# Kernel tuning notes

Measured on AMD Instinct MI355X. Metric: run time of the kernel, lower is better.

Reference implementation:

```python
import jax, jax.numpy as jnp
import numpy as np
import math
from jax import lax

BATCH, SEQ_LEN, ENC_IN = 8, 2048, 1
D_MODEL, N_HEADS, E_LAYERS, D_FF, FACTOR, C_OUT = 512, 8, 3, 512, 5, 2
EPS = 1e-5


def _layernorm(x, g, b):
    mu = x.mean(-1, keepdims=True)
    var = ((x - mu) ** 2).mean(-1, keepdims=True)
    return (x - mu) / jnp.sqrt(var + EPS) * g + b


def _prob_attention(q, k, v, key):
    # q,k,v: [B,H,L,Dh]; ProbSparse: sample U keys per query, pick top-u queries by M = max - mean
    B, H, L, Dh = q.shape
    U = min(FACTOR * int(np.ceil(np.log(L))), L)  # U_part == u since L_Q == L_K
    idx = jax.random.randint(key, (L, U), 0, L)   # sampled key indices per query
    k_samp = k[:, :, idx, :]                       # [B,H,L,U,Dh]
    qk = jnp.einsum('bhld,bhlud->bhlu', q, k_samp)
    M = qk.max(-1) - qk.mean(-1)                   # sparsity measure [B,H,L]
    _, top = lax.top_k(M, U)                       # active query indices [B,H,U]
    q_red = jnp.take_along_axis(q, top[..., None], axis=2)
    scores = jnp.einsum('bhud,bhkd->bhuk', q_red, k) * (1.0 / math.sqrt(Dh))
    A = jax.nn.softmax(scores, axis=-1)
    ctx = jnp.broadcast_to(v.mean(axis=2, keepdims=True), q.shape)  # lazy-query context = mean(V)
    upd = jnp.einsum('bhuk,bhkd->bhud', A, v)
    b = jnp.arange(B)[:, None, None]
    h = jnp.arange(H)[None, :, None]
    return ctx.at[b, h, top].set(upd)


def _encoder_layer(x, p, key):
    Wq, Wk, Wv, bq, bk, bv, Wo, bo, W1, b1, W2, b2, g1, be1, g2, be2 = p
    B, L, dm = x.shape
    Dh = dm // N_HEADS
    split = lambda t: t.reshape(B, L, N_HEADS, Dh).transpose(0, 2, 1, 3)
    q = split(x @ Wq.T + bq)
    k = split(x @ Wk.T + bk)
    v = split(x @ Wv.T + bv)
    o = _prob_attention(q, k, v, key).transpose(0, 2, 1, 3).reshape(B, L, dm)
    x = _layernorm(x + o @ Wo.T + bo, g1, be1)
    y = jax.nn.gelu(x @ W1.T + b1, approximate=False) @ W2.T + b2  # 1x1 convs == linears
    return _layernorm(x + y, g2, be2)


def _distil_conv(x, w, b, g, be):
    # Conv1d(dm,dm,3, circular pad) -> BatchNorm(eval) -> ELU -> MaxPool1d(3, stride 2, pad 1)
    xc = jnp.pad(x.transpose(0, 2, 1), ((0, 0), (0, 0), (1, 1)), mode='wrap')
    y = lax.conv_general_dilated(xc, w, (1,), 'VALID', dimension_numbers=('NCH', 'OIH', 'NCH'))
    y = y + b[None, :, None]
    y = y / np.float32(np.sqrt(1.0 + EPS)) * g[None, :, None] + be[None, :, None]
    y = jax.nn.elu(y)
    y = lax.reduce_window(y, -jnp.inf, lax.max, (1, 1, 3), (1, 1, 2), [(0, 0), (0, 0), (1, 1)])
    return y.transpose(0, 2, 1)


def _forward(x_enc, tok_w, Wq, Wk, Wv, bq, bk, bv, Wo, bo, W1, b1, W2, b2,
             ln1_g, ln1_b, ln2_g, ln2_b, dc_w, dc_b, bn_g, bn_b, lnf_g, lnf_b, proj_w, proj_b):
    B, L = x_enc.shape
    dm = D_MODEL
    # TokenEmbedding: circular Conv1d(1, d_model, 3, bias=False)
    xc = jnp.pad(x_enc[:, None, :], ((0, 0), (0, 0), (1, 1)), mode='wrap')
    tok = lax.conv_general_dilated(xc, tok_w, (1,), 'VALID', dimension_numbers=('NCH', 'OIH', 'NCH'))
    tok = tok.transpose(0, 2, 1)  # [B,L,dm]
    # fixed sinusoidal positional embedding
    pos = jnp.arange(L, dtype=jnp.float32)[:, None]
    div = jnp.exp(jnp.arange(0, dm, 2, dtype=jnp.float32) * (-math.log(10000.0) / dm))
    pe = jnp.zeros((L, dm), jnp.float32).at[:, 0::2].set(jnp.sin(pos * div)).at[:, 1::2].set(jnp.cos(pos * div))
    x = tok + pe[None]
    key = jax.random.key(42)
    for i in range(E_LAYERS):
        p = (Wq[i], Wk[i], Wv[i], bq[i], bk[i], bv[i], Wo[i], bo[i],
             W1[i], b1[i], W2[i], b2[i], ln1_g[i], ln1_b[i], ln2_g[i], ln2_b[i])
        x = _encoder_layer(x, p, jax.random.fold_in(key, i))
        if i < E_LAYERS - 1:
            x = _distil_conv(x, dc_w[i], dc_b[i], bn_g[i], bn_b[i])
    x = _layernorm(x, lnf_g, lnf_b)
    return x.max(axis=1) @ proj_w.T + proj_b  # [B, C_OUT]


def setup_inputs() -> dict:
    key = jax.random.key(0)
    ks = jax.random.split(key, 12)
    dm, dff, L = D_MODEL, D_FF, E_LAYERS
    w = lambda k, shape, fan: jax.random.normal(k, shape, jnp.float32) / np.float32(np.sqrt(fan))
    return {
        'x_enc': jax.random.normal(ks[0], (BATCH, SEQ_LEN), jnp.float32),
        'tok_w': w(ks[1], (dm, ENC_IN, 3), 3 * ENC_IN),
        'Wq': w(ks[2], (L, dm, dm), dm), 'Wk': w(ks[3], (L, dm, dm), dm),
        'Wv': w(ks[4], (L, dm, dm), dm), 'Wo': w(ks[5], (L, dm, dm), dm),
        'bq': jnp.zeros((L, dm)), 'bk': jnp.zeros((L, dm)),
        'bv': jnp.zeros((L, dm)), 'bo': jnp.zeros((L, dm)),
        'W1': w(ks[6], (L, dff, dm), dm), 'b1': jnp.zeros((L, dff)),
        'W2': w(ks[7], (L, dm, dff), dff), 'b2': jnp.zeros((L, dm)),
        'ln1_g': jnp.ones((L, dm)), 'ln1_b': jnp.zeros((L, dm)),
        'ln2_g': jnp.ones((L, dm)), 'ln2_b': jnp.zeros((L, dm)),
        'dc_w': w(ks[8], (L - 1, dm, dm, 3), 3 * dm), 'dc_b': jnp.zeros((L - 1, dm)),
        'bn_g': jnp.ones((L - 1, dm)), 'bn_b': jnp.zeros((L - 1, dm)),
        'lnf_g': jnp.ones((dm,)), 'lnf_b': jnp.zeros((dm,)),
        'proj_w': w(ks[9], (C_OUT, dm), dm), 'proj_b': jnp.zeros((C_OUT,)),
    }


def reference(x_enc, tok_w, Wq, Wk, Wv, bq, bk, bv, Wo, bo, W1, b1, W2, b2,
              ln1_g, ln1_b, ln2_g, ln2_b, dc_w, dc_b, bn_g, bn_b, lnf_g, lnf_b, proj_w, proj_b):
    return _forward(x_enc, tok_w, Wq, Wk, Wv, bq, bk, bv, Wo, bo, W1, b1, W2, b2,
                    ln1_g, ln1_b, ln2_g, ln2_b, dc_w, dc_b, bn_g, bn_b, lnf_g, lnf_b, proj_w, proj_b)
```

## Files before the change

kernel.cpp:

```cpp
#include <hip/hip_runtime.h>

#define B_ 8
#define H_ 8
#define DM 512
#define DH 64
#define LMAX 2048
#define COUT 2

typedef __attribute__((ext_vector_type(8))) short frag8;
typedef __attribute__((ext_vector_type(4))) float f32x4;

typedef __attribute__((address_space(1))) const unsigned int guint;
typedef __attribute__((address_space(3))) unsigned int luint;
__device__ __forceinline__ void dma16(const short* g, short* l) {
  __builtin_amdgcn_global_load_lds((guint*)g, (luint*)l, 16, 0, 0);
}

__device__ __forceinline__ short f2bf(float v) {
  unsigned u = __float_as_uint(v);
  unsigned r = (u + 0x7fffu + ((u >> 16) & 1u)) >> 16;
  return (short)r;
}
__device__ __forceinline__ float bf2f(short s) {
  return __uint_as_float(((unsigned)(unsigned short)s) << 16);
}
__device__ __forceinline__ void split3(float v, short* p0, short* p1, short* p2, size_t i) {
  short h0 = f2bf(v);
  float r1 = v - bf2f(h0);
  short h1 = f2bf(r1);
  float r2 = r1 - bf2f(h1);
  p0[i] = h0; p1[i] = h1; p2[i] = f2bf(r2);
}

__device__ __forceinline__ void tf2x32(unsigned k0, unsigned k1, unsigned x0, unsigned x1,
                                       unsigned& o0, unsigned& o1) {
  unsigned ks2 = k0 ^ k1 ^ 0x1BD11BDAu;
  x0 += k0; x1 += k1;
#define RND(r) { x0 += x1; x1 = (x1 << r) | (x1 >> (32 - r)); x1 ^= x0; }
  RND(13) RND(15) RND(26) RND(6)  x0 += k1;  x1 += ks2 + 1u;
  RND(17) RND(29) RND(16) RND(24) x0 += ks2; x1 += k0 + 2u;
  RND(13) RND(15) RND(26) RND(6)  x0 += k0;  x1 += k1 + 3u;
  RND(17) RND(29) RND(16) RND(24) x0 += k1;  x1 += ks2 + 4u;
  RND(13) RND(15) RND(26) RND(6)  x0 += ks2; x1 += k0 + 5u;
#undef RND
  o0 = x0; o1 = x1;
}

__global__ void idx_kernel(int* __restrict__ idxArr, int L, int U, int layer) {
  int p = blockIdx.x * 256 + threadIdx.x;
  int half = L * U;
  if (p >= half) return;
  unsigned fk0, fk1, k20, k21, o0, o1;
  tf2x32(0u, 42u, 0u, (unsigned)layer, fk0, fk1);
  tf2x32(fk0, fk1, 0u, 1u, k20, k21);
  tf2x32(k20, k21, 0u, (unsigned)p, o0, o1);
  idxArr[p] = (int)((o0 ^ o1) & (unsigned)(L - 1));
}

__global__ void embed_kernel(const float* __restrict__ xe, const float* __restrict__ tw,
                             float* __restrict__ X, short* __restrict__ P0,
                             short* __restrict__ P1, short* __restrict__ P2) {
  int i = blockIdx.x * 256 + threadIdx.x;
  int c = i % DM;
  int l = (i / DM) % LMAX;
  int b = i / (DM * LMAX);
  int lm = (l + LMAX - 1) & (LMAX - 1);
  int lp = (l + 1) & (LMAX - 1);
  const float* xb = xe + b * LMAX;
  float tok = tw[c * 3 + 0] * xb[lm] + tw[c * 3 + 1] * xb[l] + tw[c * 3 + 2] * xb[lp];
  float freq = expf(-(float)(c & ~1) * (9.210340371976184f / 512.0f));
  float ang = (float)l * freq;
  float pe = (c & 1) ? cosf(ang) : sinf(ang);
  float v = tok + pe;
  X[i] = v;
  split3(v, P0, P1, P2, (size_t)i);
}

__global__ void wsplit_kernel(const float* __restrict__ W, short* __restrict__ P0,
                              short* __restrict__ P1, short* __restrict__ P2, int n) {
  int i = blockIdx.x * 256 + threadIdx.x;
  if (i >= n) return;
  split3(W[i], P0, P1, P2, (size_t)i);
}

__global__ void wt3_kernel(const float* __restrict__ w, short* __restrict__ P0,
                           short* __restrict__ P1, short* __restrict__ P2) {
  int i = blockIdx.x * 256 + threadIdx.x;
  int n = i / 1536, r = i - n * 1536, tap = r >> 9, k = r & 511;
  float v = w[((size_t)n * DM + k) * 3 + tap];
  split3(v, P0, P1, P2, (size_t)i);
}

__global__ void bcat_kernel(const float* __restrict__ bq, const float* __restrict__ bk,
                            const float* __restrict__ bv, float* __restrict__ o) {
  int i = blockIdx.x * 256 + threadIdx.x;
  o[i] = i < 512 ? bq[i] : (i < 1024 ? bk[i - 512] : bv[i - 1024]);
}

template <int ACT, int QKV, int ACC, int CONV, int BN>
__global__ __launch_bounds__(256) void mgemm(const short* __restrict__ A0g,
                                             const short* __restrict__ A1g,
                                             const short* __restrict__ A2g,
                                             const short* __restrict__ W0g,
                                             const short* __restrict__ W1g,
                                             const short* __restrict__ W2g,
                                             const float* __restrict__ bias,
                                             const float* __restrict__ bng,
                                             const float* __restrict__ bnbe,
                                             float* __restrict__ C, long qs,
                                             int L, int Ktot) {
  __shared__ short A0[128 * 32], A1[128 * 32], A2[128 * 32];
  __shared__ short B0[128 * 32], B1[128 * 32], B2[128 * 32];
  int tid = threadIdx.x;
  int lane = tid & 63, wave = tid >> 6;
  int crow = lane >> 2, ckq = lane & 3;
  int gx = gridDim.x;
  int flat = blockIdx.y * gx + blockIdx.x;
  int mB, nB;
  if ((gridDim.y & 7) == 0) {
    int phase = flat & 7, sup = flat >> 3;
    nB = sup % gx;
    mB = phase + 8 * (sup / gx);
  } else {
    nB = blockIdx.x; mB = blockIdx.y;
  }
  int n0 = nB * 128, m0 = mB * 128;
  int wm = (wave >> 1) * 64, wn = (wave & 1) * 64;
  f32x4 acc[4][4] = {};
  int lrow = lane & 15, lq = lane >> 4;

  for (int k0 = 0; k0 < Ktot; k0 += 32) {
    int tap = 0, kcol = k0;
    if (CONV) { tap = k0 >> 9; kcol = k0 & 511; }
#pragma unroll
    for (int q = 0; q < 6; ++q) {
      int gc = wave * 6 + q;
      int pl = gc >> 3, c = gc & 7;
      int grow = m0 + c * 16 + crow;
      const short* gp;
      if (CONV) {
        int b = grow / L, l = grow - b * L;
        int le = l + tap - 1;
        le = (le < 0) ? le + L : (le >= L ? le - L : le);
        gp = ((size_t)(b * L + le) * DM + kcol + ckq * 8) +
             (pl == 0 ? A0g : pl == 1 ? A1g : A2g);
      } else {
        gp = ((size_t)grow * DM + k0 + ckq * 8) +
             (pl == 0 ? A0g : pl == 1 ? A1g : A2g);
      }
      short* lp = (pl == 0 ? A0 : pl == 1 ? A1 : A2) + c * 512;
      dma16(gp, lp);
    }
#pragma unroll
    for (int q = 0; q < 6; ++q) {
      int gc = wave * 6 + q;
      int pl = gc >> 3, c = gc & 7;
      int grow = n0 + c * 16 + crow;
      const short* gp = ((size_t)grow * Ktot + k0 + ckq * 8) +
                        (pl == 0 ? W0g : pl == 1 ? W1g : W2g);
      short* lp = (pl == 0 ? B0 : pl == 1 ? B1 : B2) + c * 512;
      dma16(gp, lp);
    }
    __syncthreads();
    frag8 a0f[4], a1f[4], a2f[4];
#pragma unroll
    for (int ti = 0; ti < 4; ++ti) {
      int off = (wm + ti * 16 + lrow) * 32 + lq * 8;
      a0f[ti] = *(const frag8*)&A0[off];
      a1f[ti] = *(const frag8*)&A1[off];
      a2f[ti] = *(const frag8*)&A2[off];
    }
#pragma unroll
    for (int tj = 0; tj < 4; ++tj) {
      int off = (wn + tj * 16 + lrow) * 32 + lq * 8;
      frag8 b0 = *(const frag8*)&B0[off];
      frag8 b1 = *(const frag8*)&B1[off];
      frag8 b2 = *(const frag8*)&B2[off];
#pragma unroll
      for (int ti = 0; ti < 4; ++ti) {
        f32x4 ac = acc[ti][tj];
        ac = __builtin_amdgcn_mfma_f32_16x16x32_bf16(a1f[ti], b1, ac, 0, 0, 0);
        ac = __builtin_amdgcn_mfma_f32_16x16x32_bf16(a0f[ti], b2, ac, 0, 0, 0);
        ac = __builtin_amdgcn_mfma_f32_16x16x32_bf16(a2f[ti], b0, ac, 0, 0, 0);
        ac = __builtin_amdgcn_mfma_f32_16x16x32_bf16(a0f[ti], b1, ac, 0, 0, 0);
        ac = __builtin_amdgcn_mfma_f32_16x16x32_bf16(a1f[ti], b0, ac, 0, 0, 0);
        ac = __builtin_amdgcn_mfma_f32_16x16x32_bf16(a0f[ti], b0, ac, 0, 0, 0);
        acc[ti][tj] = ac;
      }
    }
    __syncthreads();
  }
#pragma unroll
  for (int ti = 0; ti < 4; ++ti) {
#pragma unroll
    for (int tj = 0; tj < 4; ++tj) {
#pragma unroll
      for (int r = 0; r < 4; ++r) {
        int row = m0 + wm + ti * 16 + lq * 4 + r;
        int col = n0 + wn + tj * 16 + lrow;
        float v = acc[ti][tj][r];
        if (!CONV) v += bias[col];
        if (ACT) v = 0.5f * v * (1.0f + erff(v * 0.70710678118654752f));
        if (BN) {
          const float invs = 0.9999950000374997f;
          float z = v + bias[col];
          z = z * invs * bng[col] + bnbe[col];
          v = z > 0.f ? z : expm1f(z);
        }
        if (QKV) {
          int sel = col >> 9, cc = col & 511;
          int b = row / L, l = row - b * L;
          int h = cc >> 6, d = cc & 63;
          C[(size_t)sel * qs + (((size_t)b * H_ + h) * L + l) * DH + d] = v;
        } else if (ACC) {
          C[(size_t)row * DM + col] += v;
        } else {
          C[(size_t)row * DM + col] = v;
        }
      }
    }
  }
}

template <int U>
__global__ void qkM_t(const float* __restrict__ Q, const float* __restrict__ Kd,
                      const int* __restrict__ idxArr, float* __restrict__ Mout, int L) {
  int lane = threadIdx.x & 63, wv = threadIdx.x >> 6;
  int row = blockIdx.x * 4 + wv;
  int l = row % L, bh = row / L;
  int u = lane & 7, dc = lane >> 3;
  const float* Qb = Q + ((size_t)bh * L + l) * DH + dc * 8;
  float4 q0 = *(const float4*)(Qb);
  float4 q1 = *(const float4*)(Qb + 4);
  const float* Kb = Kd + (size_t)bh * L * DH;
  const int* ip = idxArr + l * U;
  const int NP = (U + 7) / 8;
  float mx = -1e30f, sm = 0.f;
#pragma unroll
  for (int p = 0; p < NP; ++p) {
    int s = p * 8 + u;
    bool valid = (s < U);
    int ki = ip[valid ? s : 0];
    const float* kr = Kb + (size_t)ki * DH + dc * 8;
    float4 k0 = *(const float4*)(kr);
    float4 k1 = *(const float4*)(kr + 4);
    float d = q0.x * k0.x + q0.y * k0.y + q0.z * k0.z + q0.w * k0.w +
              q1.x * k1.x + q1.y * k1.y + q1.z * k1.z + q1.w * k1.w;
    d += __shfl_xor(d, 8, 64);
    d += __shfl_xor(d, 16, 64);
    d += __shfl_xor(d, 32, 64);
    if (valid) { mx = fmaxf(mx, d); sm += d; }
  }
#pragma unroll
  for (int o = 1; o <= 4; o <<= 1) {
    mx = fmaxf(mx, __shfl_xor(mx, o, 64));
    sm += __shfl_xor(sm, o, 64);
  }
  if (lane == 0) Mout[row] = mx - sm / (float)U;
}

__global__ void topk_kernel(const float* __restrict__ M, int* __restrict__ top, int L, int U) {
  __shared__ float vals[LMAX];
  __shared__ float wvv[4];
  __shared__ int wii[4];
  int bh = blockIdx.x, tid = threadIdx.x, lane = tid & 63, w = tid >> 6;
  for (int j = tid; j < L; j += 256) vals[j] = M[(size_t)bh * L + j];
  __syncthreads();
  for (int u = 0; u < U; ++u) {
    float bv = -1e30f; int bi = L;
    for (int j = tid; j < L; j += 256) {
      float v = vals[j];
      if (v > bv) { bv = v; bi = j; }
    }
#pragma unroll
    for (int o = 32; o >= 1; o >>= 1) {
      float ov = __shfl_xor(bv, o, 64);
      int oi = __shfl_xor(bi, o, 64);
      if (ov > bv || (ov == bv && oi < bi)) { bv = ov; bi = oi; }
    }
    if (lane == 0) { wvv[w] = bv; wii[w] = bi; }
    __syncthreads();
    if (tid == 0) {
#pragma unroll
      for (int k = 1; k < 4; ++k) {
        if (wvv[k] > bv || (wvv[k] == bv && wii[k] < bi)) { bv = wvv[k]; bi = wii[k]; }
      }
      top[bh * U + u] = bi;
      vals[bi] = -1e30f;
    }
    __syncthreads();
  }
}

__global__ void vmean_kernel(const float* __restrict__ V, float* __restrict__ VM, int L) {
  __shared__ float red[256];
  int bh = blockIdx.x, tid = threadIdx.x, d = tid & 63, sq = tid >> 6;
  float s = 0.f;
  for (int l = sq; l < L; l += 4) s += V[((size_t)bh * L + l) * DH + d];
  red[tid] = s;
  __syncthreads();
  if (sq == 0) VM[bh * DH + d] = (red[d] + red[d + 64] + red[d + 128] + red[d + 192]) / (float)L;
}

__global__ void fill_kernel(const float* __restrict__ VM, short* __restrict__ P0,
                            short* __restrict__ P1, short* __restrict__ P2, int L) {
  size_t i = (size_t)blockIdx.x * 256 + threadIdx.x;
  int c = (int)(i % DM);
  int b = (int)(i / ((size_t)L * DM));
  split3(VM[b * DM + c], P0, P1, P2, i);
}

__global__ __launch_bounds__(512) void attn_fused(const float* __restrict__ Q,
                                                  const float* __restrict__ Kd,
                                                  const float* __restrict__ V,
                                                  const int* __restrict__ top,
                                                  short* __restrict__ OP0,
                                                  short* __restrict__ OP1,
                                                  short* __restrict__ OP2,
                                                  int L, int U) {
  __shared__ float Qs[8][64];
  __shared__ float Kt[64][65];
  __shared__ float Vs[64][68];
  __shared__ float ps[8][64];
  __shared__ int lst[8];
  int nch = (U + 7) >> 3;
  int bh = blockIdx.x / nch, ch = blockIdx.x - bh * nch;
  int u0g = ch * 8;
  int qn = U - u0g; if (qn > 8) qn = 8;
  int tid = threadIdx.x, lane = tid & 63, wv = tid >> 6;
  if (tid < qn) lst[tid] = top[bh * U + u0g + tid];
  __syncthreads();
  if (tid < qn * 64) {
    int u = tid >> 6, d = tid & 63;
    Qs[u][d] = Q[((size_t)bh * L + lst[u]) * DH + d];
  }
  __syncthreads();
  int ua = wv;
  bool hasA = ua < qn;
  float m0 = -1e30f, l0 = 0.f, o0 = 0.f;
  const float* Kbase = Kd + (size_t)bh * L * DH;
  const float* Vbase = V + (size_t)bh * L * DH;
  for (int t0 = 0; t0 < L; t0 += 64) {
#pragma unroll
    for (int it = 0; it < 2; ++it) {
      int idx = tid + it * 512;
      int j = idx >> 4, d4 = (idx & 15) * 4;
      float4 kv = *(const float4*)(Kbase + (size_t)(t0 + j) * DH + d4);
      Kt[d4 + 0][j] = kv.x; Kt[d4 + 1][j] = kv.y;
      Kt[d4 + 2][j] = kv.z; Kt[d4 + 3][j] = kv.w;
      *(float4*)&Vs[j][d4] = *(const float4*)(Vbase + (size_t)(t0 + j) * DH + d4);
    }
    __syncthreads();
    float s0 = 0.f;
#pragma unroll 16
    for (int d = 0; d < 64; ++d) {
      float kd = Kt[d][lane];
      s0 += kd * Qs[ua & 7][d];
    }
    s0 *= 0.125f;
    if (hasA) {
      float tm = s0;
#pragma unroll
      for (int o = 32; o >= 1; o >>= 1) tm = fmaxf(tm, __shfl_xor(tm, o, 64));
      float nm = fmaxf(m0, tm);
      float alpha = expf(m0 - nm);
      float p = expf(s0 - nm);
      float tsum = p;
#pragma unroll
      for (int o = 32; o >= 1; o >>= 1) tsum += __shfl_xor(tsum, o, 64);
      l0 = l0 * alpha + tsum;
      m0 = nm;
      ps[ua][lane] = p;
      o0 *= alpha;
#pragma unroll 16
      for (int j = 0; j < 64; ++j) o0 += ps[ua][j] * Vs[j][lane];
    }
    __syncthreads();
  }
  int b = bh / H_, h = bh - b * H_;
  if (hasA) {
    size_t i = ((size_t)b * L + lst[ua]) * DM + h * DH + lane;
    split3(o0 / l0, OP0, OP1, OP2, i);
  }
}

__global__ void ln_kernel(float* __restrict__ X, const float* __restrict__ g,
                          const float* __restrict__ be, short* __restrict__ P0,
                          short* __restrict__ P1, short* __restrict__ P2) {
  __shared__ float red[256];
  int row = blockIdx.x, tid = threadIdx.x;
  size_t base = (size_t)row * DM;
  float t0 = X[base + tid];
  float t1 = X[base + tid + 256];
  red[tid] = t0 + t1;
  __syncthreads();
  for (int s = 128; s >= 1; s >>= 1) { if (tid < s) red[tid] += red[tid + s]; __syncthreads(); }
  float mu = red[0] / 512.0f;
  __syncthreads();
  float d0 = t0 - mu, d1 = t1 - mu;
  red[tid] = d0 * d0 + d1 * d1;
  __syncthreads();
  for (int s = 128; s >= 1; s >>= 1) { if (tid < s) red[tid] += red[tid + s]; __syncthreads(); }
  float rstd = 1.0f / sqrtf(red[0] / 512.0f + 1e-5f);
  float v0 = d0 * rstd * g[tid] + be[tid];
  float v1 = d1 * rstd * g[tid + 256] + be[tid + 256];
  X[base + tid] = v0;
  X[base + tid + 256] = v1;
  if (P0) {
    split3(v0, P0, P1, P2, base + tid);
    split3(v1, P0, P1, P2, base + tid + 256);
  }
}

__global__ void pool_kernel(const float* __restrict__ Y, float* __restrict__ X, int L2,
                            short* __restrict__ P0, short* __restrict__ P1,
                            short* __restrict__ P2) {
  int i = blockIdx.x * 256 + threadIdx.x;
  int c = i % DM;
  int t = (i / DM) % L2;
  int b = i / (DM * L2);
  int L = L2 * 2;
  const float* yb = Y + (size_t)b * L * DM + c;
  float m = fmaxf(yb[(size_t)(2 * t) * DM], yb[(size_t)(2 * t + 1) * DM]);
  if (t > 0) m = fmaxf(m, yb[(size_t)(2 * t - 1) * DM]);
  X[i] = m;
  split3(m, P0, P1, P2, (size_t)i);
}

__global__ void colmax1_kernel(const float* __restrict__ X, float* __restrict__ P, int L) {
  int nlc = L >> 6;
  int bl = blockIdx.x;
  int b = bl / nlc, lc = bl % nlc;
  const float* xb = X + ((size_t)b * L + lc * 64) * DM;
  for (int c = threadIdx.x; c < DM; c += 256) {
    float m = -1e30f;
    for (int r = 0; r < 64; ++r) m = fmaxf(m, xb[(size_t)r * DM + c]);
    P[((size_t)b * nlc + lc) * DM + c] = m;
  }
}
__global__ void colmax2_kernel(const float* __restrict__ P, float* __restrict__ mc, int nlc) {
  int i = blockIdx.x * 256 + threadIdx.x;
  int b = i / DM, c = i % DM;
  float m = -1e30f;
  for (int lc = 0; lc < nlc; ++lc) m = fmaxf(m, P[((size_t)b * nlc + lc) * DM + c]);
  mc[i] = m;
}

__global__ void proj_kernel(const float* __restrict__ mc, const float* __restrict__ pw,
                            const float* __restrict__ pb, float* __restrict__ out) {
  __shared__ float red[256];
  int bo = blockIdx.x, b = bo / COUT, o = bo % COUT, tid = threadIdx.x;
  float s = mc[b * DM + tid] * pw[o * DM + tid] +
            mc[b * DM + tid + 256] * pw[o * DM + tid + 256];
  red[tid] = s;
  __syncthreads();
  for (int st = 128; st >= 1; st >>= 1) { if (tid < st) red[tid] += red[tid + st]; __syncthreads(); }
  if (tid == 0) out[bo] = red[0] + pb[o];
}

extern "C" void kernel_launch(void* const* d_in, const int* in_sizes, int n_in,
                              void* d_out, int out_size, void* d_ws, size_t ws_size,
                              hipStream_t stream) {
  (void)in_sizes; (void)n_in; (void)out_size;
  const float* xe   = (const float*)d_in[0];
  const float* tw   = (const float*)d_in[1];
  const float* Wq   = (const float*)d_in[2];
  const float* Wk   = (const float*)d_in[3];
  const float* Wv   = (const float*)d_in[4];
  const float* Wo   = (const float*)d_in[5];
  const float* bq   = (const float*)d_in[6];
  const float* bk   = (const float*)d_in[7];
  const float* bv   = (const float*)d_in[8];
  const float* bo   = (const float*)d_in[9];
  const float* W1   = (const float*)d_in[10];
  const float* b1   = (const float*)d_in[11];
  const float* W2   = (const float*)d_in[12];
  const float* b2   = (const float*)d_in[13];
  const float* ln1g = (const float*)d_in[14];
  const float* ln1b = (const float*)d_in[15];
  const float* ln2g = (const float*)d_in[16];
  const float* ln2b = (const float*)d_in[17];
  const float* dcw  = (const float*)d_in[18];
  const float* dcb  = (const float*)d_in[19];
  const float* bng  = (const float*)d_in[20];
  const float* bnb  = (const float*)d_in[21];
  const float* lnfg = (const float*)d_in[22];
  const float* lnfb = (const float*)d_in[23];
  const float* pw   = (const float*)d_in[24];
  const float* pb   = (const float*)d_in[25];
  float* out = (float*)d_out;

  float* Wf = (float*)d_ws;
  const size_t NB  = (size_t)B_ * LMAX * DM;
  const size_t NHB = (size_t)H_ * LMAX * DH;
  const size_t S_IDX = 81920, S_MV = 131072, S_TOP = 4096, S_VM = 4096,
               S_MC = 4096, S_BC = 2048, S_P = 32768;
  const size_t PLANE  = (size_t)512 * 1536;
  const size_t APLANE = NB;
  const size_t S_WP = 3 * PLANE / 2 + 1024;
  const size_t S_AP = 3 * APLANE / 2 + 1024;
  const size_t SMALL = S_IDX + S_MV + S_TOP + S_VM + S_MC + S_BC + S_P + S_WP + S_AP + 1024;

  int g = 8;
  while (g > 1 && (2 * NB + 3 * (size_t)g * NHB + SMALL) * 4 > ws_size) g >>= 1;

  float* X  = Wf;
  float* T  = X + NB;
  float* Q  = T + NB;
  float* K  = Q + (size_t)g * NHB;
  float* V  = K + (size_t)g * NHB;
  float* SM = V + (size_t)g * NHB;
  int*   IDX = (int*)SM;
  float* Mv  = SM + S_IDX;
  int*   TOP = (int*)(Mv + S_MV);
  float* VM  = Mv + S_MV + S_TOP;
  float* MC  = VM + S_VM;
  float* BCAT = MC + S_MC;
  float* P   = BCAT + S_BC;
  short* WP0 = (short*)(P + S_P);
  short* WP1 = WP0 + PLANE;
  short* WP2 = WP1 + PLANE;
  short* AP0 = (short*)((float*)(P + S_P) + S_WP);
  short* AP1 = AP0 + APLANE;
  short* AP2 = AP1 + APLANE;

  embed_kernel<<<B_ * LMAX * DM / 256, 256, 0, stream>>>(xe, tw, X, AP0, AP1, AP2);

  int L = LMAX;
  for (int i = 0; i < 3; ++i) {
    int U = (i == 0) ? 40 : 35;
    size_t wOff = (size_t)i * DM * DM;
    int ng = B_ / g;
    int nch = (U + 7) >> 3;
    const int NW = DM * DM;

    idx_kernel<<<(L * U + 255) / 256, 256, 0, stream>>>(IDX, L, U, i);

    for (int gb = 0; gb < ng; ++gb) {
      size_t aoff = (size_t)gb * g * L * DM;
      bcat_kernel<<<6, 256, 0, stream>>>(bq + i * DM, bk + i * DM, bv + i * DM, BCAT);
      wsplit_kernel<<<NW / 256, 256, 0, stream>>>(Wq + wOff, WP0, WP1, WP2, NW);
      wsplit_kernel<<<NW / 256, 256, 0, stream>>>(Wk + wOff, WP0 + NW, WP1 + NW,
                                                  WP2 + NW, NW);
      wsplit_kernel<<<NW / 256, 256, 0, stream>>>(Wv + wOff, WP0 + 2 * NW, WP1 + 2 * NW,
                                                  WP2 + 2 * NW, NW);
      dim3 gq3(1536 / 128, g * L / 128);
      mgemm<0, 1, 0, 0, 0><<<gq3, 256, 0, stream>>>(
          AP0 + aoff, AP1 + aoff, AP2 + aoff, WP0, WP1, WP2, BCAT, nullptr, nullptr,
          Q, (long)((size_t)g * NHB), L, DM);
      if (U == 40) qkM_t<40><<<g * H_ * L / 4, 256, 0, stream>>>(Q, K, IDX, Mv, L);
      else         qkM_t<35><<<g * H_ * L / 4, 256, 0, stream>>>(Q, K, IDX, Mv, L);
      topk_kernel<<<g * H_, 256, 0, stream>>>(Mv, TOP, L, U);
      vmean_kernel<<<g * H_, 256, 0, stream>>>(V, VM, L);
      fill_kernel<<<(unsigned)((size_t)g * L * DM / 256), 256, 0, stream>>>(
          VM, AP0 + aoff, AP1 + aoff, AP2 + aoff, L);
      attn_fused<<<g * H_ * nch, 512, 0, stream>>>(Q, K, V, TOP, AP0 + aoff,
                                                   AP1 + aoff, AP2 + aoff, L, U);
    }

    int Mf = B_ * L * DM;
    dim3 gf(DM / 128, B_ * L / 128);
    wsplit_kernel<<<NW / 256, 256, 0, stream>>>(Wo + wOff, WP0, WP1, WP2, NW);
    mgemm<0, 0, 1, 0, 0><<<gf, 256, 0, stream>>>(AP0, AP1, AP2, WP0, WP1, WP2,
                                                 bo + i * DM, nullptr, nullptr,
                                                 X, 0, L, DM);
    ln_kernel<<<B_ * L, 256, 0, stream>>>(X, ln1g + i * DM, ln1b + i * DM, AP0, AP1, AP2);
    wsplit_kernel<<<NW / 256, 256, 0, stream>>>(W1 + wOff, WP0, WP1, WP2, NW);
    mgemm<1, 0, 0, 0, 0><<<gf, 256, 0, stream>>>(AP0, AP1, AP2, WP0, WP1, WP2,
                                                 b1 + i * DM, nullptr, nullptr,
                                                 T, 0, L, DM);
    wsplit_kernel<<<Mf / 256, 256, 0, stream>>>(T, AP0, AP1, AP2, Mf);
    wsplit_kernel<<<NW / 256, 256, 0, stream>>>(W2 + wOff, WP0, WP1, WP2, NW);
    mgemm<0, 0, 1, 0, 0><<<gf, 256, 0, stream>>>(AP0, AP1, AP2, WP0, WP1, WP2,
                                                 b2 + i * DM, nullptr, nullptr,
                                                 X, 0, L, DM);
    if (i < 2) {
      ln_kernel<<<B_ * L, 256, 0, stream>>>(X, ln2g + i * DM, ln2b + i * DM, AP0, AP1, AP2);
      wt3_kernel<<<DM * 1536 / 256, 256, 0, stream>>>(dcw + (size_t)i * DM * DM * 3,
                                                      WP0, WP1, WP2);
      mgemm<0, 0, 0, 1, 1><<<gf, 256, 0, stream>>>(AP0, AP1, AP2, WP0, WP1, WP2,
                                                   dcb + i * DM, bng + i * DM,
                                                   bnb + i * DM, T, 0, L, 1536);
      L >>= 1;
      pool_kernel<<<B_ * L * DM / 256, 256, 0, stream>>>(T, X, L, AP0, AP1, AP2);
    } else {
      ln_kernel<<<B_ * L, 256, 0, stream>>>(X, ln2g + i * DM, ln2b + i * DM,
                                            nullptr, nullptr, nullptr);
    }
  }

  ln_kernel<<<B_ * L, 256, 0, stream>>>(X, lnfg, lnfb, nullptr, nullptr, nullptr);
  colmax1_kernel<<<B_ * (L >> 6), 256, 0, stream>>>(X, P, L);
  colmax2_kernel<<<B_ * DM / 256, 256, 0, stream>>>(P, MC, L >> 6);
  proj_kernel<<<B_ * COUT, 256, 0, stream>>>(MC, pw, pb, out);
}
```

Baseline: 2.167 ms.

## Fuse FFN split into GEMM epilogue, merge QKV weight prep, prefetch attention K/V

The FFN1 GEMM now writes its GELU output straight into the three bf16 split planes, reusing the Q buffer as storage. This removes the separate fp32 T write and the full-activation wsplit pass. The QKV weight split and bias concat are merged into one kernel and hoisted out of the batch-group loop, so they run once per layer. The attention kernel register-prefetches the next K/V tile while computing on the current one. The risk is that reusing the Q buffer for FFN planes assumes Q is dead and large enough at that point.

Result: no change. 2.135 ms (-1.5%).

```diff
diff --git a/kernel.cpp b/kernel.cpp
--- a/kernel.cpp
+++ b/kernel.cpp
@@ -83,6 +83,22 @@
   split3(W[i], P0, P1, P2, (size_t)i);
 }
 
+__global__ void wqkv_kernel(const float* __restrict__ Wq, const float* __restrict__ Wk,
+                            const float* __restrict__ Wv, const float* __restrict__ bq,
+                            const float* __restrict__ bk, const float* __restrict__ bv,
+                            short* __restrict__ P0, short* __restrict__ P1,
+                            short* __restrict__ P2, float* __restrict__ bcat) {
+  int i = blockIdx.x * 256 + threadIdx.x;
+  int n = i >> 9, k = i & 511;
+  int sel = n >> 9, nn = n & 511;
+  const float* W = sel == 0 ? Wq : sel == 1 ? Wk : Wv;
+  split3(W[(size_t)nn * 512 + k], P0, P1, P2, (size_t)i);
+  if (i < 1536) {
+    const float* bs = i < 512 ? bq : i < 1024 ? bk : bv;
+    bcat[i] = bs[i & 511];
+  }
+}
+
 __global__ void wt3_kernel(const float* __restrict__ w, short* __restrict__ P0,
                            short* __restrict__ P1, short* __restrict__ P2) {
   int i = blockIdx.x * 256 + threadIdx.x;
@@ -91,13 +107,7 @@
   split3(v, P0, P1, P2, (size_t)i);
 }
 
-__global__ void bcat_kernel(const float* __restrict__ bq, const float* __restrict__ bk,
-                            const float* __restrict__ bv, float* __restrict__ o) {
-  int i = blockIdx.x * 256 + threadIdx.x;
-  o[i] = i < 512 ? bq[i] : (i < 1024 ? bk[i - 512] : bv[i - 1024]);
-}
-
-template <int ACT, int QKV, int ACC, int CONV, int BN>
+template <int ACT, int QKV, int ACC, int CONV, int BN, int SOUT>
 __global__ __launch_bounds__(256) void mgemm(const short* __restrict__ A0g,
                                              const short* __restrict__ A1g,
                                              const short* __restrict__ A2g,
@@ -107,6 +117,9 @@
                                              const float* __restrict__ bias,
                                              const float* __restrict__ bng,
                                              const float* __restrict__ bnbe,
+                                             short* __restrict__ OP0,
+                                             short* __restrict__ OP1,
+                                             short* __restrict__ OP2,
                                              float* __restrict__ C, long qs,
                                              int L, int Ktot) {
   __shared__ short A0[128 * 32], A1[128 * 32], A2[128 * 32];
@@ -207,7 +220,9 @@
           z = z * invs * bng[col] + bnbe[col];
           v = z > 0.f ? z : expm1f(z);
         }
-        if (QKV) {
+        if (SOUT) {
+          split3(v, OP0, OP1, OP2, (size_t)row * DM + col);
+        } else if (QKV) {
           int sel = col >> 9, cc = col & 511;
           int b = row / L, l = row - b * L;
           int h = cc >> 6, d = cc & 63;
@@ -340,17 +355,27 @@
   float m0 = -1e30f, l0 = 0.f, o0 = 0.f;
   const float* Kbase = Kd + (size_t)bh * L * DH;
   const float* Vbase = V + (size_t)bh * L * DH;
+  int j0 = tid >> 4, d40 = (tid & 15) * 4;
+  int j1 = j0 + 32;
+  float4 kra = *(const float4*)(Kbase + (size_t)j0 * DH + d40);
+  float4 vra = *(const float4*)(Vbase + (size_t)j0 * DH + d40);
+  float4 krb = *(const float4*)(Kbase + (size_t)j1 * DH + d40);
+  float4 vrb = *(const float4*)(Vbase + (size_t)j1 * DH + d40);
   for (int t0 = 0; t0 < L; t0 += 64) {
-#pragma unroll
-    for (int it = 0; it < 2; ++it) {
-      int idx = tid + it * 512;
-      int j = idx >> 4, d4 = (idx & 15) * 4;
-      float4 kv = *(const float4*)(Kbase + (size_t)(t0 + j) * DH + d4);
-      Kt[d4 + 0][j] = kv.x; Kt[d4 + 1][j] = kv.y;
-      Kt[d4 + 2][j] = kv.z; Kt[d4 + 3][j] = kv.w;
-      *(float4*)&Vs[j][d4] = *(const float4*)(Vbase + (size_t)(t0 + j) * DH + d4);
-    }
+    Kt[d40 + 0][j0] = kra.x; Kt[d40 + 1][j0] = kra.y;
+    Kt[d40 + 2][j0] = kra.z; Kt[d40 + 3][j0] = kra.w;
+    *(float4*)&Vs[j0][d40] = vra;
+    Kt[d40 + 0][j1] = krb.x; Kt[d40 + 1][j1] = krb.y;
+    Kt[d40 + 2][j1] = krb.z; Kt[d40 + 3][j1] = krb.w;
+    *(float4*)&Vs[j1][d40] = vrb;
     __syncthreads();
+    if (t0 + 64 < L) {
+      kra = *(const float4*)(Kbase + (size_t)(t0 + 64 + j0) * DH + d40);
+      vra = *(const float4*)(Vbase + (size_t)(t0 + 64 + j0) * DH + d40);
+      krb = *(const float4*)(Kbase + (size_t)(t0 + 64 + j1) * DH + d40);
+      vrb = *(const float4*)(Vbase + (size_t)(t0 + 64 + j1) * DH + d40);
+    }
+    __builtin_amdgcn_sched_barrier(0);
     float s0 = 0.f;
 #pragma unroll 16
     for (int d = 0; d < 64; ++d) {
@@ -523,6 +548,9 @@
   short* AP0 = (short*)((float*)(P + S_P) + S_WP);
   short* AP1 = AP0 + APLANE;
   short* AP2 = AP1 + APLANE;
+  short* FP0 = (short*)Q;
+  short* FP1 = FP0 + APLANE;
+  short* FP2 = FP1 + APLANE;
 
   embed_kernel<<<B_ * LMAX * DM / 256, 256, 0, stream>>>(xe, tw, X, AP0, AP1, AP2);
 
@@ -535,19 +563,16 @@
     const int NW = DM * DM;
 
     idx_kernel<<<(L * U + 255) / 256, 256, 0, stream>>>(IDX, L, U, i);
+    wqkv_kernel<<<3 * NW / 256, 256, 0, stream>>>(Wq + wOff, Wk + wOff, Wv + wOff,
+                                                  bq + i * DM, bk + i * DM, bv + i * DM,
+                                                  WP0, WP1, WP2, BCAT);
 
     for (int gb = 0; gb < ng; ++gb) {
       size_t aoff = (size_t)gb * g * L * DM;
-      bcat_kernel<<<6, 256, 0, stream>>>(bq + i * DM, bk + i * DM, bv + i * DM, BCAT);
-      wsplit_kernel<<<NW / 256, 256, 0, stream>>>(Wq + wOff, WP0, WP1, WP2, NW);
-      wsplit_kernel<<<NW / 256, 256, 0, stream>>>(Wk + wOff, WP0 + NW, WP1 + NW,
-                                                  WP2 + NW, NW);
-      wsplit_kernel<<<NW / 256, 256, 0, stream>>>(Wv + wOff, WP0 + 2 * NW, WP1 + 2 * NW,
-                                                  WP2 + 2 * NW, NW);
       dim3 gq3(1536 / 128, g * L / 128);
-      mgemm<0, 1, 0, 0, 0><<<gq3, 256, 0, stream>>>(
+      mgemm<0, 1, 0, 0, 0, 0><<<gq3, 256, 0, stream>>>(
           AP0 + aoff, AP1 + aoff, AP2 + aoff, WP0, WP1, WP2, BCAT, nullptr, nullptr,
-          Q, (long)((size_t)g * NHB), L, DM);
+          nullptr, nullptr, nullptr, Q, (long)((size_t)g * NHB), L, DM);
       if (U == 40) qkM_t<40><<<g * H_ * L / 4, 256, 0, stream>>>(Q, K, IDX, Mv, L);
       else         qkM_t<35><<<g * H_ * L / 4, 256, 0, stream>>>(Q, K, IDX, Mv, L);
       topk_kernel<<<g * H_, 256, 0, stream>>>(Mv, TOP, L, U);
@@ -558,29 +583,28 @@
                                                    AP1 + aoff, AP2 + aoff, L, U);
     }
 
-    int Mf = B_ * L * DM;
     dim3 gf(DM / 128, B_ * L / 128);
     wsplit_kernel<<<NW / 256, 256, 0, stream>>>(Wo + wOff, WP0, WP1, WP2, NW);
-    mgemm<0, 0, 1, 0, 0><<<gf, 256, 0, stream>>>(AP0, AP1, AP2, WP0, WP1, WP2,
-                                                 bo + i * DM, nullptr, nullptr,
-                                                 X, 0, L, DM);
+    mgemm<0, 0, 1, 0, 0, 0><<<gf, 256, 0, stream>>>(AP0, AP1, AP2, WP0, WP1, WP2,
+                                                    bo + i * DM, nullptr, nullptr,
+                                                    nullptr, nullptr, nullptr, X, 0, L, DM);
     ln_kernel<<<B_ * L, 256, 0, stream>>>(X, ln1g + i * DM, ln1b + i * DM, AP0, AP1, AP2);
     wsplit_kernel<<<NW / 256, 256, 0, stream>>>(W1 + wOff, WP0, WP1, WP2, NW);
-    mgemm<1, 0, 0, 0, 0><<<gf, 256, 0, stream>>>(AP0, AP1, AP2, WP0, WP1, WP2,
-                                                 b1 + i * DM, nullptr, nullptr,
-                                                 T, 0, L, DM);
-    wsplit_kernel<<<Mf / 256, 256, 0, stream>>>(T, AP0, AP1, AP2, Mf);
+    mgemm<1, 0, 0, 0, 0, 1><<<gf, 256, 0, stream>>>(AP0, AP1, AP2, WP0, WP1, WP2,
+                                                    b1 + i * DM, nullptr, nullptr,
+                                                    FP0, FP1, FP2, nullptr, 0, L, DM);
     wsplit_kernel<<<NW / 256, 256, 0, stream>>>(W2 + wOff, WP0, WP1, WP2, NW);
-    mgemm<0, 0, 1, 0, 0><<<gf, 256, 0, stream>>>(AP0, AP1, AP2, WP0, WP1, WP2,
-                                                 b2 + i * DM, nullptr, nullptr,
-                                                 X, 0, L, DM);
+    mgemm<0, 0, 1, 0, 0, 0><<<gf, 256, 0, stream>>>(FP0, FP1, FP2, WP0, WP1, WP2,
+                                                    b2 + i * DM, nullptr, nullptr,
+                                                    nullptr, nullptr, nullptr, X, 0, L, DM);
     if (i < 2) {
       ln_kernel<<<B_ * L, 256, 0, stream>>>(X, ln2g + i * DM, ln2b + i * DM, AP0, AP1, AP2);
       wt3_kernel<<<DM * 1536 / 256, 256, 0, stream>>>(dcw + (size_t)i * DM * DM * 3,
                                                       WP0, WP1, WP2);
-      mgemm<0, 0, 0, 1, 1><<<gf, 256, 0, stream>>>(AP0, AP1, AP2, WP0, WP1, WP2,
-                                                   dcb + i * DM, bng + i * DM,
-                                                   bnb + i * DM, T, 0, L, 1536);
+      mgemm<0, 0, 0, 1, 1, 0><<<gf, 256, 0, stream>>>(AP0, AP1, AP2, WP0, WP1, WP2,
+                                                      dcb + i * DM, bng + i * DM,
+                                                      bnb + i * DM, nullptr, nullptr,
+                                                      nullptr, T, 0, L, 1536);
       L >>= 1;
       pool_kernel<<<B_ * L * DM / 256, 256, 0, stream>>>(T, X, L, AP0, AP1, AP2);
     } else {
```
